# Performance work log

Hardware: AMD Instinct MI355X
Metric: run time of the kernel (lower is better)

The kernel has to match this reference:

```python
import jax, jax.numpy as jnp
import numpy as np

N_BINS = 15
DELTA = 1.0 / N_BINS


def setup_inputs() -> dict:
    key = jax.random.key(0)
    k1, k2 = jax.random.split(key)
    N, C = 4_000_000, 10
    # scale 5 -> confident softmax -> low collision entropy so bins [0,1) are populated
    logits = jax.random.normal(k1, (N, C), dtype=jnp.float32) * 5.0
    labels = jax.random.randint(k2, (N,), 0, C)
    return {"logits": logits, "labels": labels}


def reference(logits, labels):
    # probs: [N, C]
    probs = jax.nn.softmax(logits, axis=-1)
    # collision entropy H2 per sample: [N]
    u = -jnp.log2(jnp.sum(probs * probs, axis=-1) + 1e-12)
    err_real = (jnp.argmax(probs, axis=-1) != labels).astype(jnp.float32)  # [N]

    n = u.shape[0]
    # bin b covers [b*DELTA, (b+1)*DELTA); samples with u outside [0,1) go to overflow bin
    bin_idx = jnp.floor(u / DELTA).astype(jnp.int32)
    valid = (u >= 0.0) & (u < 1.0)
    seg = jnp.where(valid, bin_idx, N_BINS)

    vf = valid.astype(jnp.float32)
    counts = jax.ops.segment_sum(vf, seg, num_segments=N_BINS + 1)[:N_BINS]
    sum_u = jax.ops.segment_sum(jnp.where(valid, u, 0.0), seg, num_segments=N_BINS + 1)[:N_BINS]
    sum_err = jax.ops.segment_sum(jnp.where(valid, err_real, 0.0), seg, num_segments=N_BINS + 1)[:N_BINS]

    pi = counts / n                      # population weight per bin
    nonempty = counts > 0
    cnt = jnp.where(nonempty, counts, 1.0)
    u_b = sum_u / cnt                    # mean H2 in bin
    err_b = sum_err / cnt                # empirical error rate in bin

    # risk-from-H2 reference curve
    inner = jnp.clip(2.0 * jnp.exp2(-u_b) - 1.0, 0.0, None)
    r_ref = 0.5 * (1.0 - jnp.sqrt(inner))

    gaps = jnp.where(nonempty, jnp.abs(err_b - r_ref) * pi, 0.0)
    return jnp.sum(gaps)
```

## Files before the change

kernel.cpp:

```cpp
#include <hip/hip_runtime.h>
#include <math.h>

#define NB 15


__device__ __forceinline__ void row_stats(const float lv[10], int lab, int N_ok,
                                          int& bin, float& u, int& e10)
{
    float m = lv[0];
#pragma unroll
    for (int j = 1; j < 10; ++j) m = fmaxf(m, lv[j]);

    const float c = 1.44269504088896340736f;
    float mc = m * c;
    float Z = 0.0f, S = 0.0f;
#pragma unroll
    for (int j = 0; j < 10; ++j) {
        float e = exp2f(fmaf(lv[j], c, -mc));
        Z += e;
        S = fmaf(e, e, S);
    }
    float ratio = S * __builtin_amdgcn_rcpf(Z * Z);
    u = -log2f(ratio + 1e-12f);

    bool valid = N_ok && (u >= 0.0f) && (u < 1.0f);
    bin = -1;
    if (valid) {
        bin = (int)(u * 15.0f);
        if (bin > 14) bin = 14;
    }
    if (!valid) u = 0.0f;

    float lvl = lv[0];
#pragma unroll
    for (int j = 1; j < 10; ++j) lvl = (lab == j) ? lv[j] : lvl;
    e10 = (lvl != m) ? 1 : 0;
}

__global__ __launch_bounds__(256, 4) void bin_kernel(
    const float* __restrict__ logits,
    const int* __restrict__ labels,
    float* __restrict__ acc,
    int N)
{
    __shared__ float s_acc[3 * NB];
    const int t = threadIdx.x;
    if (t < 3 * NB) s_acc[t] = 0.0f;

    int   pk[NB];
    float su[NB];
#pragma unroll
    for (int b = 0; b < NB; ++b) { pk[b] = 0; su[b] = 0.0f; }

    const float2* __restrict__ src2 = (const float2*)logits;
    const int stride = gridDim.x * 256;
    int r = blockIdx.x * 256 + t;

    for (; r + stride < N; r += 2 * stride) {
        const int r2i = r + stride;
        float a[10], b2[10];
        {
            const float2* p = src2 + (long long)r * 5;
#pragma unroll
            for (int j = 0; j < 5; ++j) { float2 w = p[j]; a[2*j] = w.x; a[2*j+1] = w.y; }
        }
        {
            const float2* p = src2 + (long long)r2i * 5;
#pragma unroll
            for (int j = 0; j < 5; ++j) { float2 w = p[j]; b2[2*j] = w.x; b2[2*j+1] = w.y; }
        }
        int labA = labels[r];
        int labB = labels[r2i];

        int binA, eA, binB, eB;
        float uA, uB;
        row_stats(a,  labA, 1, binA, uA, eA);
        row_stats(b2, labB, 1, binB, uB, eB);

        int incA = 1 + (eA << 16);
        int incB = 1 + (eB << 16);
#pragma unroll
        for (int b = 0; b < NB; ++b) {
            bool mA = (binA == b);
            bool mB = (binB == b);
            pk[b] += (mA ? incA : 0) + (mB ? incB : 0);
            su[b] += (mA ? uA : 0.0f) + (mB ? uB : 0.0f);
        }
    }
    if (r < N) {
        float a[10];
        const float2* p = src2 + (long long)r * 5;
#pragma unroll
        for (int j = 0; j < 5; ++j) { float2 w = p[j]; a[2*j] = w.x; a[2*j+1] = w.y; }
        int lab = labels[r];
        int bin, e10; float u;
        row_stats(a, lab, 1, bin, u, e10);
        int inc = 1 + (e10 << 16);
#pragma unroll
        for (int b = 0; b < NB; ++b) {
            bool mt = (bin == b);
            pk[b] += mt ? inc : 0;
            su[b] += mt ? u : 0.0f;
        }
    }

    const int lane = t & 63;
#pragma unroll
    for (int b = 0; b < NB; ++b) {
        int   p = pk[b];
        float s = su[b];
#pragma unroll
        for (int off = 1; off < 64; off <<= 1) {
            p += __shfl_xor(p, off, 64);
            s += __shfl_xor(s, off, 64);
        }
        if (lane == 0) {
            atomicAdd(&s_acc[b],          (float)(p & 0xFFFF));
            atomicAdd(&s_acc[NB + b],     s);
            atomicAdd(&s_acc[2 * NB + b], (float)(p >> 16));
        }
    }
    __syncthreads();
    if (t < 3 * NB) {
        float v = s_acc[t];
        if (v != 0.0f) atomicAdd(&acc[t], v);
    }
}

__global__ void finalize_kernel(const float* __restrict__ acc,
                                float* __restrict__ out, float n)
{
    int b = threadIdx.x;
    float gap = 0.0f;
    if (b < NB) {
        float cnt = acc[b];
        if (cnt > 0.0f) {
            float u_b   = acc[NB + b] / cnt;
            float err_b = acc[2 * NB + b] / cnt;
            float inner = 2.0f * exp2f(-u_b) - 1.0f;
            if (inner < 0.0f) inner = 0.0f;
            float r_ref = 0.5f * (1.0f - sqrtf(inner));
            gap = fabsf(err_b - r_ref) * (cnt / n);
        }
    }
#pragma unroll
    for (int off = 32; off >= 1; off >>= 1)
        gap += __shfl_xor(gap, off, 64);
    if (b == 0) out[0] = gap;
}

extern "C" void kernel_launch(void* const* d_in, const int* in_sizes, int n_in,
                              void* d_out, int out_size, void* d_ws, size_t ws_size,
                              hipStream_t stream)
{
    const float* logits = (const float*)d_in[0];
    const int*   labels = (const int*)d_in[1];
    const int N = in_sizes[1];

    float* acc = (float*)d_ws;
    hipMemsetAsync(acc, 0, 3 * NB * sizeof(float), stream);

    int blocks = 2048;
    int maxBlocks = (N + 255) / 256;
    if (blocks > maxBlocks) blocks = maxBlocks;
    bin_kernel<<<blocks, 256, 0, stream>>>(logits, labels, acc, N);
    finalize_kernel<<<1, 64, 0, stream>>>(acc, (float*)d_out, (float)N);
}
```

Before: 265.0 us.

## Stage logits tiles into LDS with direct global-to-LDS loads and spread atomics

Each block now processes 512-row tiles, loading them into shared memory with coalesced 16-byte global_load_lds instructions instead of strided per-thread float2 loads, then reading rows from LDS. The label logit is taken by indexing LDS rather than with a select chain. Global atomics are spread across 8 accumulator copies that the finalize kernel sums. Each tile adds two barriers and no double-buffering, so load latency is not overlapped within a block and relies on occupancy.

```diff
diff --git a/kernel.cpp b/kernel.cpp
--- a/kernel.cpp
+++ b/kernel.cpp
@@ -1,10 +1,23 @@
 #include <hip/hip_runtime.h>
 #include <math.h>
+#include <stdint.h>
 
 #define NB 15
+#define TROWS 512
+#define TBYTES (TROWS * 40)
+#define NCOPY 8
+#define ACCSTRIDE 64
 
 
-__device__ __forceinline__ void row_stats(const float lv[10], int lab, int N_ok,
+__device__ __forceinline__ void gload_lds16(const void* g, float* ldsBase, uint32_t ldsByteOff)
+{
+    __builtin_amdgcn_global_load_lds(
+        (const __attribute__((address_space(1))) uint32_t*)g,
+        (__attribute__((address_space(3))) uint32_t*)((char*)ldsBase + ldsByteOff),
+        16, 0, 0);
+}
+
+__device__ __forceinline__ void row_stats(const float lv[10], float lvl_lab, bool rowOK,
                                           int& bin, float& u, int& e10)
 {
     float m = lv[0];
@@ -23,59 +36,74 @@
     float ratio = S * __builtin_amdgcn_rcpf(Z * Z);
     u = -log2f(ratio + 1e-12f);
 
-    bool valid = N_ok && (u >= 0.0f) && (u < 1.0f);
+    bool valid = rowOK && (u >= 0.0f) && (u < 1.0f);
     bin = -1;
     if (valid) {
         bin = (int)(u * 15.0f);
         if (bin > 14) bin = 14;
     }
     if (!valid) u = 0.0f;
-
-    float lvl = lv[0];
-#pragma unroll
-    for (int j = 1; j < 10; ++j) lvl = (lab == j) ? lv[j] : lvl;
-    e10 = (lvl != m) ? 1 : 0;
+    e10 = (lvl_lab != m) ? 1 : 0;
 }
 
-__global__ __launch_bounds__(256, 4) void bin_kernel(
+__global__ __launch_bounds__(256) void bin_kernel(
     const float* __restrict__ logits,
     const int* __restrict__ labels,
     float* __restrict__ acc,
-    int N)
+    int N, int numTiles)
 {
+    __shared__ float lds[TROWS * 10];
     __shared__ float s_acc[3 * NB];
+
     const int t = threadIdx.x;
     if (t < 3 * NB) s_acc[t] = 0.0f;
+    const int wid  = t >> 6;
+    const int lane = t & 63;
 
     int   pk[NB];
     float su[NB];
 #pragma unroll
     for (int b = 0; b < NB; ++b) { pk[b] = 0; su[b] = 0.0f; }
 
-    const float2* __restrict__ src2 = (const float2*)logits;
-    const int stride = gridDim.x * 256;
-    int r = blockIdx.x * 256 + t;
+    const char* srcB = (const char*)logits;
+    const long long totB = (long long)N * 40;
 
-    for (; r + stride < N; r += 2 * stride) {
-        const int r2i = r + stride;
+    for (int tile = blockIdx.x; tile < numTiles; tile += gridDim.x) {
+        const long long tb = (long long)tile * TBYTES;
+
+        const int r0 = tile * TROWS + t;
+        const int r1 = r0 + 256;
+        const int lab0 = (r0 < N) ? labels[r0] : 0;
+        const int lab1 = (r1 < N) ? labels[r1] : 0;
+
+        __syncthreads();
+#pragma unroll
+        for (int k = 0; k < 5; ++k) {
+            uint32_t loff = (uint32_t)(wid * 5 + k) << 10;
+            long long gb = tb + loff + lane * 16;
+            if (gb < totB)
+                gload_lds16(srcB + gb, lds, __builtin_amdgcn_readfirstlane(loff));
+        }
+        __syncthreads();
+
         float a[10], b2[10];
         {
-            const float2* p = src2 + (long long)r * 5;
+            const float2* p = (const float2*)(lds + t * 10);
 #pragma unroll
             for (int j = 0; j < 5; ++j) { float2 w = p[j]; a[2*j] = w.x; a[2*j+1] = w.y; }
         }
         {
-            const float2* p = src2 + (long long)r2i * 5;
+            const float2* p = (const float2*)(lds + (t + 256) * 10);
 #pragma unroll
             for (int j = 0; j < 5; ++j) { float2 w = p[j]; b2[2*j] = w.x; b2[2*j+1] = w.y; }
         }
-        int labA = labels[r];
-        int labB = labels[r2i];
+        float lvl0 = lds[t * 10 + lab0];
+        float lvl1 = lds[(t + 256) * 10 + lab1];
 
         int binA, eA, binB, eB;
         float uA, uB;
-        row_stats(a,  labA, 1, binA, uA, eA);
-        row_stats(b2, labB, 1, binB, uB, eB);
+        row_stats(a,  lvl0, r0 < N, binA, uA, eA);
+        row_stats(b2, lvl1, r1 < N, binB, uB, eB);
 
         int incA = 1 + (eA << 16);
         int incB = 1 + (eB << 16);
@@ -87,24 +115,7 @@
             su[b] += (mA ? uA : 0.0f) + (mB ? uB : 0.0f);
         }
     }
-    if (r < N) {
-        float a[10];
-        const float2* p = src2 + (long long)r * 5;
-#pragma unroll
-        for (int j = 0; j < 5; ++j) { float2 w = p[j]; a[2*j] = w.x; a[2*j+1] = w.y; }
-        int lab = labels[r];
-        int bin, e10; float u;
-        row_stats(a, lab, 1, bin, u, e10);
-        int inc = 1 + (e10 << 16);
-#pragma unroll
-        for (int b = 0; b < NB; ++b) {
-            bool mt = (bin == b);
-            pk[b] += mt ? inc : 0;
-            su[b] += mt ? u : 0.0f;
-        }
-    }
 
-    const int lane = t & 63;
 #pragma unroll
     for (int b = 0; b < NB; ++b) {
         int   p = pk[b];
@@ -123,7 +134,8 @@
     __syncthreads();
     if (t < 3 * NB) {
         float v = s_acc[t];
-        if (v != 0.0f) atomicAdd(&acc[t], v);
+        if (v != 0.0f)
+            atomicAdd(&acc[(blockIdx.x & (NCOPY - 1)) * ACCSTRIDE + t], v);
     }
 }
 
@@ -133,10 +145,16 @@
     int b = threadIdx.x;
     float gap = 0.0f;
     if (b < NB) {
-        float cnt = acc[b];
+        float cnt = 0.0f, sumu = 0.0f, serr = 0.0f;
+#pragma unroll
+        for (int c = 0; c < NCOPY; ++c) {
+            cnt  += acc[c * ACCSTRIDE + b];
+            sumu += acc[c * ACCSTRIDE + NB + b];
+            serr += acc[c * ACCSTRIDE + 2 * NB + b];
+        }
         if (cnt > 0.0f) {
-            float u_b   = acc[NB + b] / cnt;
-            float err_b = acc[2 * NB + b] / cnt;
+            float u_b   = sumu / cnt;
+            float err_b = serr / cnt;
             float inner = 2.0f * exp2f(-u_b) - 1.0f;
             if (inner < 0.0f) inner = 0.0f;
             float r_ref = 0.5f * (1.0f - sqrtf(inner));
@@ -158,11 +176,10 @@
     const int N = in_sizes[1];
 
     float* acc = (float*)d_ws;
-    hipMemsetAsync(acc, 0, 3 * NB * sizeof(float), stream);
+    hipMemsetAsync(acc, 0, NCOPY * ACCSTRIDE * sizeof(float), stream);
 
-    int blocks = 2048;
-    int maxBlocks = (N + 255) / 256;
-    if (blocks > maxBlocks) blocks = maxBlocks;
-    bin_kernel<<<blocks, 256, 0, stream>>>(logits, labels, acc, N);
+    const int numTiles = (N + TROWS - 1) / TROWS;
+    int blocks = numTiles < 1792 ? numTiles : 1792;
+    bin_kernel<<<blocks, 256, 0, stream>>>(logits, labels, acc, N, numTiles);
     finalize_kernel<<<1, 64, 0, stream>>>(acc, (float*)d_out, (float)N);
 }
```

New measurement: 245.9 us. 1.08x faster.
